# Optimization experiments

Hardware: AMD Instinct MI355X
Metric: run time of the kernel (lower is better)

Reference implementation:

```python
import jax, jax.numpy as jnp
import numpy as np

N_NODES = 100000
IN_DIM = 64
HID = 64
N_EDGES = 1600000
EPS = 1e-5
SLOPE = 0.01  # F.leaky_relu default


def _glorot(key, shape):
    fan_in, fan_out = shape[1], shape[0]
    lim = jnp.sqrt(6.0 / (fan_in + fan_out))
    return jax.random.uniform(key, shape, jnp.float32, -lim, lim)


def setup_inputs() -> dict:
    key = jax.random.key(0)
    ks = jax.random.split(key, 8)
    x = jax.random.normal(ks[0], (N_NODES, IN_DIM), jnp.float32)
    src = jax.random.randint(ks[1], (N_EDGES,), 0, N_NODES, jnp.int32)
    dst = jax.random.randint(ks[2], (N_EDGES,), 0, N_NODES, jnp.int32)
    edge_index = jnp.stack([src, dst])  # [2, E]
    return {
        "x": x,
        "edge_index": edge_index,
        "W_self1": _glorot(ks[3], (HID, IN_DIM)),
        "W_neigh1": _glorot(ks[4], (HID, IN_DIM)),
        "b1": jnp.zeros((HID,), jnp.float32),
        "gamma1": jnp.ones((HID,), jnp.float32),
        "beta1": jnp.zeros((HID,), jnp.float32),
        "W_self2": _glorot(ks[5], (HID, HID)),
        "W_neigh2": _glorot(ks[6], (HID, HID)),
        "b2": jnp.zeros((HID,), jnp.float32),
        "gamma2": jnp.ones((HID,), jnp.float32),
        "beta2": jnp.zeros((HID,), jnp.float32),
    }


def _sage_mean(h, src, dst, W_self, W_neigh, b):
    # neighbor mean aggregation: mean of src features at each dst node
    msg_sum = jax.ops.segment_sum(h[src], dst, num_segments=N_NODES)  # [N, d]
    deg = jax.ops.segment_sum(jnp.ones_like(dst, jnp.float32), dst, num_segments=N_NODES)
    h_neigh = msg_sum / jnp.maximum(deg, 1.0)[:, None]  # isolated nodes -> 0
    return h @ W_self.T + h_neigh @ W_neigh.T + b


def _bn(h, gamma, beta):
    mu = jnp.mean(h, axis=0)
    var = jnp.mean(jnp.square(h - mu), axis=0)
    return (h - mu) * jax.lax.rsqrt(var + EPS) * gamma + beta


def reference(x, edge_index, W_self1, W_neigh1, b1, gamma1, beta1,
              W_self2, W_neigh2, b2, gamma2, beta2):
    src, dst = edge_index[0], edge_index[1]
    h = _sage_mean(x, src, dst, W_self1, W_neigh1, b1)
    h = jax.nn.leaky_relu(_bn(h, gamma1, beta1), SLOPE)
    h = _sage_mean(h, src, dst, W_self2, W_neigh2, b2)
    h = jax.nn.leaky_relu(_bn(h, gamma2, beta2), SLOPE)
    return h
```

## Files before the change

### kernel.cpp

```cpp
#include <hip/hip_runtime.h>

#define EPS 1e-5f
#define SLOPE 0.01f

typedef short bf16x8 __attribute__((ext_vector_type(8)));
typedef float f32x4 __attribute__((ext_vector_type(4)));

static __device__ __forceinline__ unsigned short f2bf(float f) {
  unsigned u = __float_as_uint(f);
  unsigned r = (u + 0x7FFFu + ((u >> 16) & 1u)) >> 16;
  return (unsigned short)r;
}


__global__ __launch_bounds__(1024) void hist_kernel(const int* __restrict__ dst,
                                                    int* __restrict__ hist,
                                                    int E, int NB) {
  extern __shared__ int lh[];
  for (int i = threadIdx.x; i < NB; i += blockDim.x) lh[i] = 0;
  __syncthreads();
  int stride = gridDim.x * blockDim.x;
  for (int i = blockIdx.x * blockDim.x + threadIdx.x; i < E; i += stride)
    atomicAdd(&lh[((unsigned)dst[i]) >> 8], 1);
  __syncthreads();
  for (int b = threadIdx.x; b < NB; b += blockDim.x)
    hist[(size_t)b * gridDim.x + blockIdx.x] = lh[b];
}

__global__ void scan_blk(const int* in, int* out, int* bsum, int n) {
  __shared__ int s[256];
  int i = blockIdx.x * 256 + threadIdx.x;
  int v = (i < n) ? in[i] : 0;
  s[threadIdx.x] = v;
  __syncthreads();
  for (int off = 1; off < 256; off <<= 1) {
    int t = (threadIdx.x >= off) ? s[threadIdx.x - off] : 0;
    __syncthreads();
    s[threadIdx.x] += t;
    __syncthreads();
  }
  if (i < n) out[i] = s[threadIdx.x] - v;
  if (threadIdx.x == 255) bsum[blockIdx.x] = s[255];
}

__global__ void scan_top(int* bsum, int nb) {
  __shared__ int s[512];
  int tid = threadIdx.x;
  int v = (tid < nb) ? bsum[tid] : 0;
  s[tid] = v;
  __syncthreads();
  for (int off = 1; off < 512; off <<= 1) {
    int t = (tid >= off) ? s[tid - off] : 0;
    __syncthreads();
    s[tid] += t;
    __syncthreads();
  }
  if (tid < nb) bsum[tid] = s[tid] - v;
}

__global__ void scan_add(int* out, const int* bsum, int n) {
  int i = blockIdx.x * 256 + threadIdx.x;
  if (i < n) out[i] += bsum[blockIdx.x];
}

__global__ __launch_bounds__(1024) void scatter_kernel(
    const int* __restrict__ src, const int* __restrict__ dst,
    const int* __restrict__ histS, unsigned* __restrict__ binned, int E, int NB) {
  extern __shared__ int cur[];
  for (int b = threadIdx.x; b < NB; b += blockDim.x)
    cur[b] = histS[(size_t)b * gridDim.x + blockIdx.x];
  __syncthreads();
  int stride = gridDim.x * blockDim.x;
  for (int i = blockIdx.x * blockDim.x + threadIdx.x; i < E; i += stride) {
    int d = dst[i];
    unsigned s = (unsigned)src[i];
    int b = ((unsigned)d) >> 8;
    int pos = atomicAdd(&cur[b], 1);
    binned[pos] = s | (((unsigned)d & 255u) << 20);
  }
}

__global__ __launch_bounds__(256) void fine_kernel(
    const unsigned* __restrict__ binned, const int* __restrict__ histS,
    int* __restrict__ rowptr, int* __restrict__ col, int E, int NB, int NBLKB, int N) {
  __shared__ int ldeg[256];
  __shared__ int lcur[256];
  __shared__ int ss[256];
  int b = blockIdx.x;
  int tid = threadIdx.x;
  int seg_s = histS[(size_t)b * NBLKB];
  int seg_e = (b + 1 < NB) ? histS[(size_t)(b + 1) * NBLKB] : E;
  ldeg[tid] = 0;
  __syncthreads();
  for (int i = seg_s + tid; i < seg_e; i += 256)
    atomicAdd(&ldeg[(binned[i] >> 20) & 255u], 1);
  __syncthreads();
  int d = ldeg[tid];
  ss[tid] = d;
  __syncthreads();
  for (int off = 1; off < 256; off <<= 1) {
    int t = (tid >= off) ? ss[tid - off] : 0;
    __syncthreads();
    ss[tid] += t;
    __syncthreads();
  }
  int base = seg_s + ss[tid] - d;
  lcur[tid] = base;
  int node = (b << 8) + tid;
  if (node < N) rowptr[node] = base;
  __syncthreads();
  for (int i = seg_s + tid; i < seg_e; i += 256) {
    unsigned v = binned[i];
    int pos = atomicAdd(&lcur[(v >> 20) & 255u], 1);
    col[pos] = (int)(v & 0xFFFFFu);
  }
}

__global__ void sentinel_kernel(int* rowptr, int N, int E) {
  rowptr[N] = E;
}


__global__ void cvt_kernel(const float* __restrict__ x, unsigned short* __restrict__ xb,
                           int total4) {
  int stride = gridDim.x * blockDim.x;
  for (int i = blockIdx.x * blockDim.x + threadIdx.x; i < total4; i += stride) {
    float4 v = reinterpret_cast<const float4*>(x)[i];
    ushort4 o;
    o.x = f2bf(v.x); o.y = f2bf(v.y); o.z = f2bf(v.z); o.w = f2bf(v.w);
    reinterpret_cast<ushort4*>(xb)[i] = o;
  }
}


__global__ __launch_bounds__(256) void agg_kernel(
    const unsigned short* __restrict__ hb, const int* __restrict__ rowptr,
    const int* __restrict__ col, unsigned short* __restrict__ hm, int n) {
  int t = blockIdx.x * blockDim.x + threadIdx.x;
  int node = t >> 4;
  int fo = (t & 15) * 4;
  if (node >= n) return;
  int beg = rowptr[node];
  int end = rowptr[node + 1];
  float s0 = 0.f, s1 = 0.f, s2 = 0.f, s3 = 0.f;
  int e = beg;
  for (; e + 4 <= end; e += 4) {
    int i0 = col[e], i1 = col[e + 1], i2 = col[e + 2], i3 = col[e + 3];
    uint2 u0 = *reinterpret_cast<const uint2*>(&hb[(size_t)i0 * 64 + fo]);
    uint2 u1 = *reinterpret_cast<const uint2*>(&hb[(size_t)i1 * 64 + fo]);
    uint2 u2 = *reinterpret_cast<const uint2*>(&hb[(size_t)i2 * 64 + fo]);
    uint2 u3 = *reinterpret_cast<const uint2*>(&hb[(size_t)i3 * 64 + fo]);
    s0 += __uint_as_float(u0.x << 16) + __uint_as_float(u1.x << 16)
        + __uint_as_float(u2.x << 16) + __uint_as_float(u3.x << 16);
    s1 += __uint_as_float(u0.x & 0xFFFF0000u) + __uint_as_float(u1.x & 0xFFFF0000u)
        + __uint_as_float(u2.x & 0xFFFF0000u) + __uint_as_float(u3.x & 0xFFFF0000u);
    s2 += __uint_as_float(u0.y << 16) + __uint_as_float(u1.y << 16)
        + __uint_as_float(u2.y << 16) + __uint_as_float(u3.y << 16);
    s3 += __uint_as_float(u0.y & 0xFFFF0000u) + __uint_as_float(u1.y & 0xFFFF0000u)
        + __uint_as_float(u2.y & 0xFFFF0000u) + __uint_as_float(u3.y & 0xFFFF0000u);
  }
  for (; e < end; ++e) {
    uint2 u = *reinterpret_cast<const uint2*>(&hb[(size_t)col[e] * 64 + fo]);
    s0 += __uint_as_float(u.x << 16);
    s1 += __uint_as_float(u.x & 0xFFFF0000u);
    s2 += __uint_as_float(u.y << 16);
    s3 += __uint_as_float(u.y & 0xFFFF0000u);
  }
  int deg = end - beg;
  float inv = 1.0f / (float)(deg > 0 ? deg : 1);
  ushort4 o;
  o.x = f2bf(s0 * inv); o.y = f2bf(s1 * inv);
  o.z = f2bf(s2 * inv); o.w = f2bf(s3 * inv);
  *reinterpret_cast<ushort4*>(&hm[(size_t)node * 64 + fo]) = o;
}


__global__ __launch_bounds__(256) void gemm_stream(
    const unsigned short* __restrict__ A0,
    const unsigned short* __restrict__ A1,
    const float* __restrict__ Wself, const float* __restrict__ Wneigh,
    const float* __restrict__ bias,
    float* __restrict__ z, float* __restrict__ partial, int n, int ntiles) {
  int tid = threadIdx.x;
  int lane = tid & 63;
  int w = tid >> 6;
  int l15 = lane & 15;
  int g = lane >> 4;

  bf16x8 B[4][4];
  #pragma unroll
  for (int t = 0; t < 4; ++t) {
    #pragma unroll
    for (int s = 0; s < 4; ++s) {
      const float* base = (s < 2 ? Wself : Wneigh) + (t * 16 + l15) * 64 + (s & 1) * 32 + g * 8;
      float4 w0 = *reinterpret_cast<const float4*>(base);
      float4 w1 = *reinterpret_cast<const float4*>(base + 4);
      bf16x8 b;
      b[0] = (short)f2bf(w0.x); b[1] = (short)f2bf(w0.y);
      b[2] = (short)f2bf(w0.z); b[3] = (short)f2bf(w0.w);
      b[4] = (short)f2bf(w1.x); b[5] = (short)f2bf(w1.y);
      b[6] = (short)f2bf(w1.z); b[7] = (short)f2bf(w1.w);
      B[t][s] = b;
    }
  }
  float bv[4];
  #pragma unroll
  for (int t = 0; t < 4; ++t) bv[t] = bias[t * 16 + l15];

  float ps[4] = {0.f, 0.f, 0.f, 0.f};
  float pq[4] = {0.f, 0.f, 0.f, 0.f};

  int nw = gridDim.x * 4;
  for (int tile = blockIdx.x * 4 + w; tile < ntiles; tile += nw) {
    int r0 = tile * 16 + l15;
    uint4 a[4];
    if (r0 < n) {
      const uint4* pa0 = reinterpret_cast<const uint4*>(A0 + (size_t)r0 * 64);
      const uint4* pa1 = reinterpret_cast<const uint4*>(A1 + (size_t)r0 * 64);
      a[0] = pa0[g]; a[1] = pa0[4 + g]; a[2] = pa1[g]; a[3] = pa1[4 + g];
    } else {
      a[0] = a[1] = a[2] = a[3] = make_uint4(0u, 0u, 0u, 0u);
    }
    f32x4 acc[4] = {};
    #pragma unroll
    for (int s = 0; s < 4; ++s) {
      bf16x8 af = *reinterpret_cast<bf16x8*>(&a[s]);
      #pragma unroll
      for (int t = 0; t < 4; ++t)
        acc[t] = __builtin_amdgcn_mfma_f32_16x16x32_bf16(af, B[t][s], acc[t], 0, 0, 0);
    }
    #pragma unroll
    for (int t = 0; t < 4; ++t) {
      #pragma unroll
      for (int i = 0; i < 4; ++i) {
        int gr = tile * 16 + g * 4 + i;
        if (gr < n) {
          float v = acc[t][i] + bv[t];
          z[(size_t)gr * 64 + t * 16 + l15] = v;
          ps[t] += v;
          pq[t] += v * v;
        }
      }
    }
  }

  #pragma unroll
  for (int t = 0; t < 4; ++t) {
    ps[t] += __shfl_xor(ps[t], 16); ps[t] += __shfl_xor(ps[t], 32);
    pq[t] += __shfl_xor(pq[t], 16); pq[t] += __shfl_xor(pq[t], 32);
  }
  __shared__ float sred[128];
  if (tid < 128) sred[tid] = 0.f;
  __syncthreads();
  if (lane < 16) {
    #pragma unroll
    for (int t = 0; t < 4; ++t) {
      atomicAdd(&sred[t * 16 + l15], ps[t]);
      atomicAdd(&sred[64 + t * 16 + l15], pq[t]);
    }
  }
  __syncthreads();
  if (tid < 128) partial[(size_t)blockIdx.x * 128 + tid] = sred[tid];
}

__global__ __launch_bounds__(256) void reduce_stats(const float* __restrict__ partial,
                                                    float* __restrict__ stats, int nblk) {
  int f = blockIdx.x;
  float s = 0.f;
  for (int j = threadIdx.x; j < nblk; j += 256) s += partial[(size_t)j * 128 + f];
  #pragma unroll
  for (int o = 1; o < 64; o <<= 1) s += __shfl_xor(s, o);
  __shared__ float r[4];
  if ((threadIdx.x & 63) == 0) r[threadIdx.x >> 6] = s;
  __syncthreads();
  if (threadIdx.x == 0) stats[f] = r[0] + r[1] + r[2] + r[3];
}


__global__ void bn_bf16_kernel(const float* __restrict__ z, const float* __restrict__ stats,
                               const float* __restrict__ gamma, const float* __restrict__ beta,
                               unsigned short* __restrict__ out, int n) {
  __shared__ float sc[64];
  __shared__ float sh[64];
  if (threadIdx.x < 64) {
    int f = threadIdx.x;
    float invN = 1.0f / (float)n;
    float mu = stats[f] * invN;
    float var = stats[64 + f] * invN - mu * mu;
    float s = rsqrtf(var + EPS) * gamma[f];
    sc[f] = s;
    sh[f] = beta[f] - mu * s;
  }
  __syncthreads();
  int total = n * 16;
  int stride = gridDim.x * blockDim.x;
  for (int idx = blockIdx.x * blockDim.x + threadIdx.x; idx < total; idx += stride) {
    int f0 = (idx & 15) * 4;
    float4 v = reinterpret_cast<const float4*>(z)[idx];
    float t;
    ushort4 o;
    t = v.x * sc[f0 + 0] + sh[f0 + 0]; o.x = f2bf(t > 0.f ? t : SLOPE * t);
    t = v.y * sc[f0 + 1] + sh[f0 + 1]; o.y = f2bf(t > 0.f ? t : SLOPE * t);
    t = v.z * sc[f0 + 2] + sh[f0 + 2]; o.z = f2bf(t > 0.f ? t : SLOPE * t);
    t = v.w * sc[f0 + 3] + sh[f0 + 3]; o.w = f2bf(t > 0.f ? t : SLOPE * t);
    reinterpret_cast<ushort4*>(out)[idx] = o;
  }
}

__global__ void bn_f32_kernel(const float* __restrict__ z, const float* __restrict__ stats,
                              const float* __restrict__ gamma, const float* __restrict__ beta,
                              float* __restrict__ out, int n) {
  __shared__ float sc[64];
  __shared__ float sh[64];
  if (threadIdx.x < 64) {
    int f = threadIdx.x;
    float invN = 1.0f / (float)n;
    float mu = stats[f] * invN;
    float var = stats[64 + f] * invN - mu * mu;
    float s = rsqrtf(var + EPS) * gamma[f];
    sc[f] = s;
    sh[f] = beta[f] - mu * s;
  }
  __syncthreads();
  int total = n * 16;
  int stride = gridDim.x * blockDim.x;
  for (int idx = blockIdx.x * blockDim.x + threadIdx.x; idx < total; idx += stride) {
    int f0 = (idx & 15) * 4;
    float4 v = reinterpret_cast<const float4*>(z)[idx];
    float4 o;
    float t;
    t = v.x * sc[f0 + 0] + sh[f0 + 0]; o.x = t > 0.f ? t : SLOPE * t;
    t = v.y * sc[f0 + 1] + sh[f0 + 1]; o.y = t > 0.f ? t : SLOPE * t;
    t = v.z * sc[f0 + 2] + sh[f0 + 2]; o.z = t > 0.f ? t : SLOPE * t;
    t = v.w * sc[f0 + 3] + sh[f0 + 3]; o.w = t > 0.f ? t : SLOPE * t;
    reinterpret_cast<float4*>(out)[idx] = o;
  }
}


extern "C" void kernel_launch(void* const* d_in, const int* in_sizes, int n_in,
                              void* d_out, int out_size, void* d_ws, size_t ws_size,
                              hipStream_t stream) {
  const float* x  = (const float*)d_in[0];
  const int* ei   = (const int*)d_in[1];
  const float* Ws1 = (const float*)d_in[2];
  const float* Wn1 = (const float*)d_in[3];
  const float* b1  = (const float*)d_in[4];
  const float* g1  = (const float*)d_in[5];
  const float* be1 = (const float*)d_in[6];
  const float* Ws2 = (const float*)d_in[7];
  const float* Wn2 = (const float*)d_in[8];
  const float* b2  = (const float*)d_in[9];
  const float* g2  = (const float*)d_in[10];
  const float* be2 = (const float*)d_in[11];
  float* out = (float*)d_out;

  int N = in_sizes[0] / 64;
  int E = in_sizes[1] / 2;
  const int* src = ei;
  const int* dst = ei + E;

  int NB = (N + 255) >> 8;
  const int NBLKB = 256;
  int M = NB * NBLKB;

  int ntiles = (N + 15) / 16;
  int gblk = (ntiles + 7) / 8;

  char* ws = (char*)d_ws;
  float* stats1 = (float*)ws;
  float* stats2 = stats1 + 128;
  size_t off = 1024;
  auto take = [&](size_t bytes) {
    void* p = ws + off;
    off = (off + bytes + 255) & ~(size_t)255;
    return p;
  };
  int* hist   = (int*)take((size_t)M * 4);
  int* bsum   = (int*)take(512 * 4);
  int* rowptr = (int*)take((size_t)(N + 1) * 4);
  unsigned* binned = (unsigned*)take((size_t)E * 4);
  int* col    = (int*)take((size_t)E * 4);
  unsigned short* xb  = (unsigned short*)take((size_t)N * 64 * 2);
  unsigned short* hmb = (unsigned short*)take((size_t)N * 64 * 2);
  unsigned short* h1b = (unsigned short*)take((size_t)N * 64 * 2);
  float* partial = (float*)take((size_t)gblk * 128 * 4);

  hipMemsetAsync(ws, 0, 1024, stream);

  hist_kernel<<<NBLKB, 1024, NB * 4, stream>>>(dst, hist, E, NB);
  int nb1 = (M + 255) / 256;
  scan_blk<<<nb1, 256, 0, stream>>>(hist, hist, bsum, M);
  scan_top<<<1, 512, 0, stream>>>(bsum, nb1);
  scan_add<<<nb1, 256, 0, stream>>>(hist, bsum, M);
  scatter_kernel<<<NBLKB, 1024, NB * 4, stream>>>(src, dst, hist, binned, E, NB);
  fine_kernel<<<NB, 256, 0, stream>>>(binned, hist, rowptr, col, E, NB, NBLKB, N);
  sentinel_kernel<<<1, 1, 0, stream>>>(rowptr, N, E);

  cvt_kernel<<<1024, 256, 0, stream>>>(x, xb, N * 16);

  int ab = (N + 15) / 16;

  agg_kernel<<<ab, 256, 0, stream>>>(xb, rowptr, col, hmb, N);
  gemm_stream<<<gblk, 256, 0, stream>>>(xb, hmb, Ws1, Wn1, b1, out, partial, N, ntiles);
  reduce_stats<<<128, 256, 0, stream>>>(partial, stats1, gblk);
  bn_bf16_kernel<<<2048, 256, 0, stream>>>(out, stats1, g1, be1, h1b, N);

  agg_kernel<<<ab, 256, 0, stream>>>(h1b, rowptr, col, hmb, N);
  gemm_stream<<<gblk, 256, 0, stream>>>(h1b, hmb, Ws2, Wn2, b2, out, partial, N, ntiles);
  reduce_stats<<<128, 256, 0, stream>>>(partial, stats2, gblk);
  bn_f32_kernel<<<2048, 256, 0, stream>>>(out, stats2, g2, be2, out, N);
}
```

Baseline: 192.3 us.

## Fuse histogram with bf16 conversion, widen gather loads, store pre-BN activations as bf16

Merges the x-to-bf16 conversion into the histogram kernel as extra blocks and moves the rowptr sentinel write into fine_kernel, removing two launches and the workspace memset. The aggregation kernel now uses 8 threads per node with 16-byte loads instead of 16 threads with 8-byte loads. The GEMM writes the pre-BatchNorm activations as bf16 into a new workspace buffer, and the BN kernels read bf16, which halves that intermediate traffic. Batch statistics are still accumulated in fp32 before rounding, but the normalized output now carries bf16 rounding error. Dropping the memset assumes the stats regions never need zeroing, which the reduce kernel appears to overwrite anyway.

Result: faster. 173.8 us (-9.6%).

```diff
diff --git a/kernel.cpp b/kernel.cpp
--- a/kernel.cpp
+++ b/kernel.cpp
@@ -11,20 +11,34 @@
   unsigned r = (u + 0x7FFFu + ((u >> 16) & 1u)) >> 16;
   return (unsigned short)r;
 }
-
-
-__global__ __launch_bounds__(1024) void hist_kernel(const int* __restrict__ dst,
-                                                    int* __restrict__ hist,
-                                                    int E, int NB) {
+#define BFLO(u) __uint_as_float((u) << 16)
+#define BFHI(u) __uint_as_float((u) & 0xFFFF0000u)
+
+
+__global__ __launch_bounds__(1024) void hist_cvt_kernel(
+    const int* __restrict__ dst, int* __restrict__ hist, int E, int NB,
+    int histBlocks, const float* __restrict__ x, unsigned short* __restrict__ xb,
+    int total4) {
   extern __shared__ int lh[];
-  for (int i = threadIdx.x; i < NB; i += blockDim.x) lh[i] = 0;
-  __syncthreads();
-  int stride = gridDim.x * blockDim.x;
-  for (int i = blockIdx.x * blockDim.x + threadIdx.x; i < E; i += stride)
-    atomicAdd(&lh[((unsigned)dst[i]) >> 8], 1);
-  __syncthreads();
-  for (int b = threadIdx.x; b < NB; b += blockDim.x)
-    hist[(size_t)b * gridDim.x + blockIdx.x] = lh[b];
+  if ((int)blockIdx.x < histBlocks) {
+    for (int i = threadIdx.x; i < NB; i += blockDim.x) lh[i] = 0;
+    __syncthreads();
+    int stride = histBlocks * blockDim.x;
+    for (int i = blockIdx.x * blockDim.x + threadIdx.x; i < E; i += stride)
+      atomicAdd(&lh[((unsigned)dst[i]) >> 8], 1);
+    __syncthreads();
+    for (int b = threadIdx.x; b < NB; b += blockDim.x)
+      hist[(size_t)b * histBlocks + blockIdx.x] = lh[b];
+  } else {
+    int cb = blockIdx.x - histBlocks;
+    int stride = (gridDim.x - histBlocks) * blockDim.x;
+    for (int i = cb * blockDim.x + threadIdx.x; i < total4; i += stride) {
+      float4 v = reinterpret_cast<const float4*>(x)[i];
+      ushort4 o;
+      o.x = f2bf(v.x); o.y = f2bf(v.y); o.z = f2bf(v.z); o.w = f2bf(v.w);
+      reinterpret_cast<ushort4*>(xb)[i] = o;
+    }
+  }
 }
 
 __global__ void scan_blk(const int* in, int* out, int* bsum, int n) {
@@ -108,6 +122,7 @@
   lcur[tid] = base;
   int node = (b << 8) + tid;
   if (node < N) rowptr[node] = base;
+  if (b == NB - 1 && tid == 0) rowptr[N] = E;
   __syncthreads();
   for (int i = seg_s + tid; i < seg_e; i += 256) {
     unsigned v = binned[i];
@@ -116,62 +131,49 @@
   }
 }
 
-__global__ void sentinel_kernel(int* rowptr, int N, int E) {
-  rowptr[N] = E;
-}
-
-
-__global__ void cvt_kernel(const float* __restrict__ x, unsigned short* __restrict__ xb,
-                           int total4) {
-  int stride = gridDim.x * blockDim.x;
-  for (int i = blockIdx.x * blockDim.x + threadIdx.x; i < total4; i += stride) {
-    float4 v = reinterpret_cast<const float4*>(x)[i];
-    ushort4 o;
-    o.x = f2bf(v.x); o.y = f2bf(v.y); o.z = f2bf(v.z); o.w = f2bf(v.w);
-    reinterpret_cast<ushort4*>(xb)[i] = o;
-  }
-}
-
 
 __global__ __launch_bounds__(256) void agg_kernel(
     const unsigned short* __restrict__ hb, const int* __restrict__ rowptr,
     const int* __restrict__ col, unsigned short* __restrict__ hm, int n) {
-  int t = blockIdx.x * blockDim.x + threadIdx.x;
-  int node = t >> 4;
-  int fo = (t & 15) * 4;
+  int t = blockIdx.x * 256 + threadIdx.x;
+  int node = t >> 3;
+  int fo = (t & 7) * 8;
   if (node >= n) return;
   int beg = rowptr[node];
   int end = rowptr[node + 1];
   float s0 = 0.f, s1 = 0.f, s2 = 0.f, s3 = 0.f;
+  float s4 = 0.f, s5 = 0.f, s6 = 0.f, s7 = 0.f;
   int e = beg;
   for (; e + 4 <= end; e += 4) {
     int i0 = col[e], i1 = col[e + 1], i2 = col[e + 2], i3 = col[e + 3];
-    uint2 u0 = *reinterpret_cast<const uint2*>(&hb[(size_t)i0 * 64 + fo]);
-    uint2 u1 = *reinterpret_cast<const uint2*>(&hb[(size_t)i1 * 64 + fo]);
-    uint2 u2 = *reinterpret_cast<const uint2*>(&hb[(size_t)i2 * 64 + fo]);
-    uint2 u3 = *reinterpret_cast<const uint2*>(&hb[(size_t)i3 * 64 + fo]);
-    s0 += __uint_as_float(u0.x << 16) + __uint_as_float(u1.x << 16)
-        + __uint_as_float(u2.x << 16) + __uint_as_float(u3.x << 16);
-    s1 += __uint_as_float(u0.x & 0xFFFF0000u) + __uint_as_float(u1.x & 0xFFFF0000u)
-        + __uint_as_float(u2.x & 0xFFFF0000u) + __uint_as_float(u3.x & 0xFFFF0000u);
-    s2 += __uint_as_float(u0.y << 16) + __uint_as_float(u1.y << 16)
-        + __uint_as_float(u2.y << 16) + __uint_as_float(u3.y << 16);
-    s3 += __uint_as_float(u0.y & 0xFFFF0000u) + __uint_as_float(u1.y & 0xFFFF0000u)
-        + __uint_as_float(u2.y & 0xFFFF0000u) + __uint_as_float(u3.y & 0xFFFF0000u);
+    uint4 u0 = *reinterpret_cast<const uint4*>(&hb[(size_t)i0 * 64 + fo]);
+    uint4 u1 = *reinterpret_cast<const uint4*>(&hb[(size_t)i1 * 64 + fo]);
+    uint4 u2 = *reinterpret_cast<const uint4*>(&hb[(size_t)i2 * 64 + fo]);
+    uint4 u3 = *reinterpret_cast<const uint4*>(&hb[(size_t)i3 * 64 + fo]);
+    s0 += BFLO(u0.x) + BFLO(u1.x) + BFLO(u2.x) + BFLO(u3.x);
+    s1 += BFHI(u0.x) + BFHI(u1.x) + BFHI(u2.x) + BFHI(u3.x);
+    s2 += BFLO(u0.y) + BFLO(u1.y) + BFLO(u2.y) + BFLO(u3.y);
+    s3 += BFHI(u0.y) + BFHI(u1.y) + BFHI(u2.y) + BFHI(u3.y);
+    s4 += BFLO(u0.z) + BFLO(u1.z) + BFLO(u2.z) + BFLO(u3.z);
+    s5 += BFHI(u0.z) + BFHI(u1.z) + BFHI(u2.z) + BFHI(u3.z);
+    s6 += BFLO(u0.w) + BFLO(u1.w) + BFLO(u2.w) + BFLO(u3.w);
+    s7 += BFHI(u0.w) + BFHI(u1.w) + BFHI(u2.w) + BFHI(u3.w);
   }
   for (; e < end; ++e) {
-    uint2 u = *reinterpret_cast<const uint2*>(&hb[(size_t)col[e] * 64 + fo]);
-    s0 += __uint_as_float(u.x << 16);
-    s1 += __uint_as_float(u.x & 0xFFFF0000u);
-    s2 += __uint_as_float(u.y << 16);
-    s3 += __uint_as_float(u.y & 0xFFFF0000u);
+    uint4 u = *reinterpret_cast<const uint4*>(&hb[(size_t)col[e] * 64 + fo]);
+    s0 += BFLO(u.x); s1 += BFHI(u.x);
+    s2 += BFLO(u.y); s3 += BFHI(u.y);
+    s4 += BFLO(u.z); s5 += BFHI(u.z);
+    s6 += BFLO(u.w); s7 += BFHI(u.w);
   }
   int deg = end - beg;
   float inv = 1.0f / (float)(deg > 0 ? deg : 1);
-  ushort4 o;
-  o.x = f2bf(s0 * inv); o.y = f2bf(s1 * inv);
-  o.z = f2bf(s2 * inv); o.w = f2bf(s3 * inv);
-  *reinterpret_cast<ushort4*>(&hm[(size_t)node * 64 + fo]) = o;
+  uint4 o;
+  o.x = (unsigned)f2bf(s0 * inv) | ((unsigned)f2bf(s1 * inv) << 16);
+  o.y = (unsigned)f2bf(s2 * inv) | ((unsigned)f2bf(s3 * inv) << 16);
+  o.z = (unsigned)f2bf(s4 * inv) | ((unsigned)f2bf(s5 * inv) << 16);
+  o.w = (unsigned)f2bf(s6 * inv) | ((unsigned)f2bf(s7 * inv) << 16);
+  *reinterpret_cast<uint4*>(&hm[(size_t)node * 64 + fo]) = o;
 }
 
 
@@ -180,7 +182,7 @@
     const unsigned short* __restrict__ A1,
     const float* __restrict__ Wself, const float* __restrict__ Wneigh,
     const float* __restrict__ bias,
-    float* __restrict__ z, float* __restrict__ partial, int n, int ntiles) {
+    unsigned short* __restrict__ zb, float* __restrict__ partial, int n, int ntiles) {
   int tid = threadIdx.x;
   int lane = tid & 63;
   int w = tid >> 6;
@@ -236,7 +238,7 @@
         int gr = tile * 16 + g * 4 + i;
         if (gr < n) {
           float v = acc[t][i] + bv[t];
-          z[(size_t)gr * 64 + t * 16 + l15] = v;
+          zb[(size_t)gr * 64 + t * 16 + l15] = f2bf(v);
           ps[t] += v;
           pq[t] += v * v;
         }
@@ -277,7 +279,8 @@
 }
 
 
-__global__ void bn_bf16_kernel(const float* __restrict__ z, const float* __restrict__ stats,
+__global__ void bn_bf16_kernel(const unsigned short* __restrict__ zb,
+                               const float* __restrict__ stats,
                                const float* __restrict__ gamma, const float* __restrict__ beta,
                                unsigned short* __restrict__ out, int n) {
   __shared__ float sc[64];
@@ -296,18 +299,19 @@
   int stride = gridDim.x * blockDim.x;
   for (int idx = blockIdx.x * blockDim.x + threadIdx.x; idx < total; idx += stride) {
     int f0 = (idx & 15) * 4;
-    float4 v = reinterpret_cast<const float4*>(z)[idx];
+    uint2 u = reinterpret_cast<const uint2*>(zb)[idx];
     float t;
     ushort4 o;
-    t = v.x * sc[f0 + 0] + sh[f0 + 0]; o.x = f2bf(t > 0.f ? t : SLOPE * t);
-    t = v.y * sc[f0 + 1] + sh[f0 + 1]; o.y = f2bf(t > 0.f ? t : SLOPE * t);
-    t = v.z * sc[f0 + 2] + sh[f0 + 2]; o.z = f2bf(t > 0.f ? t : SLOPE * t);
-    t = v.w * sc[f0 + 3] + sh[f0 + 3]; o.w = f2bf(t > 0.f ? t : SLOPE * t);
+    t = BFLO(u.x) * sc[f0 + 0] + sh[f0 + 0]; o.x = f2bf(t > 0.f ? t : SLOPE * t);
+    t = BFHI(u.x) * sc[f0 + 1] + sh[f0 + 1]; o.y = f2bf(t > 0.f ? t : SLOPE * t);
+    t = BFLO(u.y) * sc[f0 + 2] + sh[f0 + 2]; o.z = f2bf(t > 0.f ? t : SLOPE * t);
+    t = BFHI(u.y) * sc[f0 + 3] + sh[f0 + 3]; o.w = f2bf(t > 0.f ? t : SLOPE * t);
     reinterpret_cast<ushort4*>(out)[idx] = o;
   }
 }
 
-__global__ void bn_f32_kernel(const float* __restrict__ z, const float* __restrict__ stats,
+__global__ void bn_f32_kernel(const unsigned short* __restrict__ zb,
+                              const float* __restrict__ stats,
                               const float* __restrict__ gamma, const float* __restrict__ beta,
                               float* __restrict__ out, int n) {
   __shared__ float sc[64];
@@ -326,13 +330,13 @@
   int stride = gridDim.x * blockDim.x;
   for (int idx = blockIdx.x * blockDim.x + threadIdx.x; idx < total; idx += stride) {
     int f0 = (idx & 15) * 4;
-    float4 v = reinterpret_cast<const float4*>(z)[idx];
+    uint2 u = reinterpret_cast<const uint2*>(zb)[idx];
     float4 o;
     float t;
-    t = v.x * sc[f0 + 0] + sh[f0 + 0]; o.x = t > 0.f ? t : SLOPE * t;
-    t = v.y * sc[f0 + 1] + sh[f0 + 1]; o.y = t > 0.f ? t : SLOPE * t;
-    t = v.z * sc[f0 + 2] + sh[f0 + 2]; o.z = t > 0.f ? t : SLOPE * t;
-    t = v.w * sc[f0 + 3] + sh[f0 + 3]; o.w = t > 0.f ? t : SLOPE * t;
+    t = BFLO(u.x) * sc[f0 + 0] + sh[f0 + 0]; o.x = t > 0.f ? t : SLOPE * t;
+    t = BFHI(u.x) * sc[f0 + 1] + sh[f0 + 1]; o.y = t > 0.f ? t : SLOPE * t;
+    t = BFLO(u.y) * sc[f0 + 2] + sh[f0 + 2]; o.z = t > 0.f ? t : SLOPE * t;
+    t = BFHI(u.y) * sc[f0 + 3] + sh[f0 + 3]; o.w = t > 0.f ? t : SLOPE * t;
     reinterpret_cast<float4*>(out)[idx] = o;
   }
 }
@@ -384,30 +388,27 @@
   unsigned short* xb  = (unsigned short*)take((size_t)N * 64 * 2);
   unsigned short* hmb = (unsigned short*)take((size_t)N * 64 * 2);
   unsigned short* h1b = (unsigned short*)take((size_t)N * 64 * 2);
+  unsigned short* zb  = (unsigned short*)take((size_t)N * 64 * 2);
   float* partial = (float*)take((size_t)gblk * 128 * 4);
 
-  hipMemsetAsync(ws, 0, 1024, stream);
-
-  hist_kernel<<<NBLKB, 1024, NB * 4, stream>>>(dst, hist, E, NB);
+  hist_cvt_kernel<<<NBLKB + 128, 1024, NB * 4, stream>>>(dst, hist, E, NB, NBLKB,
+                                                         x, xb, N * 16);
   int nb1 = (M + 255) / 256;
   scan_blk<<<nb1, 256, 0, stream>>>(hist, hist, bsum, M);
   scan_top<<<1, 512, 0, stream>>>(bsum, nb1);
   scan_add<<<nb1, 256, 0, stream>>>(hist, bsum, M);
   scatter_kernel<<<NBLKB, 1024, NB * 4, stream>>>(src, dst, hist, binned, E, NB);
   fine_kernel<<<NB, 256, 0, stream>>>(binned, hist, rowptr, col, E, NB, NBLKB, N);
-  sentinel_kernel<<<1, 1, 0, stream>>>(rowptr, N, E);
-
-  cvt_kernel<<<1024, 256, 0, stream>>>(x, xb, N * 16);
-
-  int ab = (N + 15) / 16;
+
+  int ab = (N * 8 + 255) / 256;
 
   agg_kernel<<<ab, 256, 0, stream>>>(xb, rowptr, col, hmb, N);
-  gemm_stream<<<gblk, 256, 0, stream>>>(xb, hmb, Ws1, Wn1, b1, out, partial, N, ntiles);
+  gemm_stream<<<gblk, 256, 0, stream>>>(xb, hmb, Ws1, Wn1, b1, zb, partial, N, ntiles);
   reduce_stats<<<128, 256, 0, stream>>>(partial, stats1, gblk);
-  bn_bf16_kernel<<<2048, 256, 0, stream>>>(out, stats1, g1, be1, h1b, N);
+  bn_bf16_kernel<<<2048, 256, 0, stream>>>(zb, stats1, g1, be1, h1b, N);
 
   agg_kernel<<<ab, 256, 0, stream>>>(h1b, rowptr, col, hmb, N);
-  gemm_stream<<<gblk, 256, 0, stream>>>(h1b, hmb, Ws2, Wn2, b2, out, partial, N, ntiles);
+  gemm_stream<<<gblk, 256, 0, stream>>>(h1b, hmb, Ws2, Wn2, b2, zb, partial, N, ntiles);
   reduce_stats<<<128, 256, 0, stream>>>(partial, stats2, gblk);
-  bn_f32_kernel<<<2048, 256, 0, stream>>>(out, stats2, g2, be2, out, N);
-}
+  bn_f32_kernel<<<2048, 256, 0, stream>>>(zb, stats2, g2, be2, out, N);
+}
```
